# Optimization experiments

Measured on AMD Instinct MI355X. Metric: run time of the kernel, lower is better.

The kernel has to match this reference:

```python
import jax, jax.numpy as jnp
import numpy as np

N_HEADS = 16

def setup_inputs() -> dict:
    key = jax.random.key(0)
    ks = jax.random.split(key, 6)
    B, L, D = 1, 2048, 1024
    M = 2048  # max_len
    dh = D // N_HEADS
    s = 0.02
    return {
        "x": jax.random.normal(ks[0], (B, L, D), jnp.float32),
        "Wqkv": jax.random.normal(ks[1], (D, 3 * D), jnp.float32) * s,
        "bqkv": jax.random.normal(ks[2], (3 * D,), jnp.float32) * s,
        "Wout": jax.random.normal(ks[3], (D, D), jnp.float32) * s,
        "bout": jax.random.normal(ks[4], (D,), jnp.float32) * s,
        "rel_emb": jax.random.normal(ks[5], (2 * M - 1, dh), jnp.float32),
    }

def reference(x, Wqkv, bqkv, Wout, bout, rel_emb):
    B, L, D = x.shape
    H = N_HEADS
    dh = D // H
    qkv = x @ Wqkv + bqkv                       # [B,L,3D]
    q, k, v = jnp.split(qkv, 3, axis=-1)
    q = q.reshape(B, L, H, dh).transpose(0, 2, 1, 3)  # [B,H,L,dh]
    k = k.reshape(B, L, H, dh).transpose(0, 2, 1, 3)
    v = v.reshape(B, L, H, dh).transpose(0, 2, 1, 3)
    content = jnp.einsum('bhid,bhjd->bhij', q, k)      # [B,H,L,L]
    rel = jnp.einsum('bhid,rd->bhir', q, rel_emb)      # [B,H,L,2M-1]
    # _skew: F.pad(x,(1,0)); view keeps shape; slice [...,:L]
    rel = jnp.pad(rel, ((0, 0), (0, 0), (0, 0), (1, 0)))[..., :L]
    scores = (content + rel) / jnp.sqrt(jnp.asarray(dh, x.dtype))
    attn = jax.nn.softmax(scores, axis=-1)
    out = jnp.einsum('bhij,bhjd->bhid', attn, v)       # [B,H,L,dh]
    out = out.transpose(0, 2, 1, 3).reshape(B, L, D)
    return out @ Wout + bout
```

## Files before the change

### kernel.cpp

```cpp
#include <hip/hip_runtime.h>
#include <hip/hip_bf16.h>
#include <stdint.h>

typedef __attribute__((ext_vector_type(8))) __bf16 bf16x8;
typedef __attribute__((ext_vector_type(4))) float f32x4;
typedef __attribute__((ext_vector_type(16))) float f32x16;
typedef __attribute__((ext_vector_type(2))) uint32_t u32x2;

#define MFMA16(a, b, c) __builtin_amdgcn_mfma_f32_16x16x32_bf16(a, b, c, 0, 0, 0)
#define MFMA32(a, b, c) __builtin_amdgcn_mfma_f32_32x32x16_bf16(a, b, c, 0, 0, 0)

typedef const __attribute__((address_space(1))) uint32_t* gas_ptr;
typedef __attribute__((address_space(3))) uint32_t* lds_ptr;

static __device__ __forceinline__ ushort f2b(float f) {
  union { float f; uint32_t u; } x; x.f = f;
  uint32_t u = x.u + 0x7fffu + ((x.u >> 16) & 1u);
  return (ushort)(u >> 16);
}

static __device__ __forceinline__ void g2lds16(const void* g, void* l) {
  __builtin_amdgcn_global_load_lds((gas_ptr)(uintptr_t)g, (lds_ptr)(uintptr_t)l, 16, 0, 0);
}

template <int N> static __device__ __forceinline__ void waitvm() {
  if constexpr (N == 0) asm volatile("s_waitcnt vmcnt(0)" ::: "memory");
  else if constexpr (N == 4) asm volatile("s_waitcnt vmcnt(4)" ::: "memory");
  else if constexpr (N == 6) asm volatile("s_waitcnt vmcnt(6)" ::: "memory");
  else if constexpr (N == 8) asm volatile("s_waitcnt vmcnt(8)" ::: "memory");
}

static __device__ __forceinline__ u32x2 plswap(uint32_t a, uint32_t b) {
  return __builtin_amdgcn_permlane32_swap(a, b, false, false);
}
static __device__ __forceinline__ float xhalf_max(float x) {
  u32x2 r = plswap(__float_as_uint(x), __float_as_uint(x));
  return fmaxf(__uint_as_float(r.x), __uint_as_float(r.y));
}
static __device__ __forceinline__ float xhalf_sum(float x) {
  u32x2 r = plswap(__float_as_uint(x), __float_as_uint(x));
  return __uint_as_float(r.x) + __uint_as_float(r.y);
}

__global__ __launch_bounds__(256) void prep(const float* __restrict__ x, ushort* __restrict__ xb,
                                            const float* __restrict__ Wqkv, ushort* __restrict__ w1t,
                                            const float* __restrict__ Wout, ushort* __restrict__ w2t,
                                            int L) {
  const int b = blockIdx.x, t = threadIdx.x;
  const int ncvt = (L * 1024) / (256 * 4);
  if (b < ncvt) {
    int i = (b * 256 + t) * 4;
    float4 v = *(const float4*)(x + i);
    ushort4 o;
    o.x = f2b(v.x); o.y = f2b(v.y); o.z = f2b(v.z); o.w = f2b(v.w);
    *(ushort4*)(xb + i) = o;
    return;
  }
  __shared__ ushort tile[64][65];
  const float* in; ushort* out; int N; int b2;
  const int K = 1024;
  if (b < ncvt + 768) { b2 = b - ncvt; N = 3072; in = Wqkv; out = w1t; }
  else                { b2 = b - ncvt - 768; N = 1024; in = Wout; out = w2t; }
  int nx = b2 % (N >> 6), ky = b2 / (N >> 6);
  int n0 = nx * 64, k0 = ky * 64;
#pragma unroll
  for (int i = 0; i < 16; ++i) {
    int idx = i * 256 + t;
    int r = idx >> 6, c = idx & 63;
    tile[r][c] = f2b(in[(size_t)(k0 + r) * N + n0 + c]);
  }
  __syncthreads();
#pragma unroll
  for (int i = 0; i < 16; ++i) {
    int idx = i * 256 + t;
    int r = idx >> 6, c = idx & 63;
    out[(size_t)(n0 + r) * K + k0 + c] = tile[c][r];
  }
}

template <int BM, int BN, bool BIAS>
__global__ __launch_bounds__(256) void gemm_dbuf(const ushort* __restrict__ A,
                                                 const ushort* __restrict__ Bt,
                                                 float* __restrict__ C,
                                                 const float* __restrict__ bias,
                                                 int M, int N, int K) {
  constexpr int WM = BM / 2, WN = BN / 2, MF = WM / 16, NF = WN / 16;
  constexpr int AI = BM / 32, BI = BN / 32;
  __shared__ ushort lA[2][BM * 64];
  __shared__ ushort lB[2][BN * 64];
  const int t = threadIdx.x, lane = t & 63;
  const int bm = blockIdx.y * BM, bn = blockIdx.x * BN;
  const int wid = t >> 6, wr = wid >> 1, wc = wid & 1;

  f32x4 acc[MF][NF] = {};

  auto STAGE = [&](int bb, int k0) {
#pragma unroll
    for (int i = 0; i < AI; ++i) {
      int ci = i * 256 + t;
      int r = ci >> 3, cs = ci & 7;
      int cg = (cs ^ (r & 7)) * 8;
      g2lds16(A + (size_t)(bm + r) * K + k0 + cg, (ushort*)lA[bb] + ci * 8);
    }
#pragma unroll
    for (int i = 0; i < BI; ++i) {
      int ci = i * 256 + t;
      int r = ci >> 3, cs = ci & 7;
      int cg = (cs ^ (r & 7)) * 8;
      g2lds16(Bt + (size_t)(bn + r) * K + k0 + cg, (ushort*)lB[bb] + ci * 8);
    }
  };

  STAGE(0, 0);
  const int NS = K >> 6;
  int buf = 0;
  for (int s = 0; s < NS; ++s) {
    if (s + 1 < NS) { STAGE(buf ^ 1, (s + 1) << 6); waitvm<AI + BI>(); }
    else            { waitvm<0>(); }
    __builtin_amdgcn_s_barrier();
    __builtin_amdgcn_sched_barrier(0);
#pragma unroll
    for (int kk = 0; kk < 2; ++kk) {
      bf16x8 af[MF], bfr[NF];
#pragma unroll
      for (int m = 0; m < MF; ++m) {
        int row = wr * WM + m * 16 + (lane & 15);
        int cb = kk * 64 + ((lane >> 4) << 4);
        int sw = cb ^ ((row & 7) << 4);
        af[m] = *(const bf16x8*)((const char*)lA[buf] + row * 128 + sw);
      }
#pragma unroll
      for (int n = 0; n < NF; ++n) {
        int row = wc * WN + n * 16 + (lane & 15);
        int cb = kk * 64 + ((lane >> 4) << 4);
        int sw = cb ^ ((row & 7) << 4);
        bfr[n] = *(const bf16x8*)((const char*)lB[buf] + row * 128 + sw);
      }
      __builtin_amdgcn_s_setprio(1);
#pragma unroll
      for (int m = 0; m < MF; ++m)
#pragma unroll
        for (int n = 0; n < NF; ++n) acc[m][n] = MFMA16(af[m], bfr[n], acc[m][n]);
      __builtin_amdgcn_s_setprio(0);
    }
    __builtin_amdgcn_s_barrier();
    __builtin_amdgcn_sched_barrier(0);
    buf ^= 1;
  }
#pragma unroll
  for (int m = 0; m < MF; ++m) {
#pragma unroll
    for (int n = 0; n < NF; ++n) {
      int col = bn + wc * WN + n * 16 + (lane & 15);
      float b = BIAS ? bias[col] : 0.f;
#pragma unroll
      for (int r = 0; r < 4; ++r) {
        int row = bm + wr * WM + m * 16 + ((lane >> 4) << 2) + r;
        C[(size_t)row * N + col] = acc[m][n][r] + b;
      }
    }
  }
}

__global__ __launch_bounds__(256) void gemm_qkv(const ushort* __restrict__ A,
                                                const ushort* __restrict__ Bt,
                                                const float* __restrict__ bqkv,
                                                const float* __restrict__ rel,
                                                ushort* __restrict__ Qs,
                                                ushort* __restrict__ Kp,
                                                ushort* __restrict__ Vt, int M) {
  __shared__ ushort lA[2][128 * 64];
  __shared__ ushort lB[2][128 * 64];
  const int K = 1024;
  const int t = threadIdx.x, lane = t & 63;
  const int bm = blockIdx.y * 128, bn = blockIdx.x * 128;
  const int wid = t >> 6, wr = wid >> 1, wc = wid & 1;

  f32x4 acc[4][4] = {};

  auto STAGE = [&](int bb, int k0) {
#pragma unroll
    for (int i = 0; i < 4; ++i) {
      int ci = i * 256 + t;
      int r = ci >> 3, cs = ci & 7;
      int cg = (cs ^ (r & 7)) * 8;
      g2lds16(A + (size_t)(bm + r) * K + k0 + cg, (ushort*)lA[bb] + ci * 8);
      g2lds16(Bt + (size_t)(bn + r) * K + k0 + cg, (ushort*)lB[bb] + ci * 8);
    }
  };

  STAGE(0, 0);
  int buf = 0;
  for (int s = 0; s < 16; ++s) {
    if (s + 1 < 16) { STAGE(buf ^ 1, (s + 1) << 6); waitvm<8>(); }
    else            { waitvm<0>(); }
    __builtin_amdgcn_s_barrier();
    __builtin_amdgcn_sched_barrier(0);
#pragma unroll
    for (int kk = 0; kk < 2; ++kk) {
      bf16x8 af[4], bfr[4];
#pragma unroll
      for (int m = 0; m < 4; ++m) {
        int row = wr * 64 + m * 16 + (lane & 15);
        int cb = kk * 64 + ((lane >> 4) << 4);
        int sw = cb ^ ((row & 7) << 4);
        af[m] = *(const bf16x8*)((const char*)lA[buf] + row * 128 + sw);
      }
#pragma unroll
      for (int n = 0; n < 4; ++n) {
        int row = wc * 64 + n * 16 + (lane & 15);
        int cb = kk * 64 + ((lane >> 4) << 4);
        int sw = cb ^ ((row & 7) << 4);
        bfr[n] = *(const bf16x8*)((const char*)lB[buf] + row * 128 + sw);
      }
      __builtin_amdgcn_s_setprio(1);
#pragma unroll
      for (int m = 0; m < 4; ++m)
#pragma unroll
        for (int n = 0; n < 4; ++n) acc[m][n] = MFMA16(af[m], bfr[n], acc[m][n]);
      __builtin_amdgcn_s_setprio(0);
    }
    __builtin_amdgcn_s_barrier();
    __builtin_amdgcn_sched_barrier(0);
    buf ^= 1;
  }

  const int sec = bn >> 10;
  const int cis_base = bn & 1023;
  if (sec < 2) {
    ushort* dst = (sec == 0) ? Qs : Kp;
    const float scale = (sec == 0) ? 0.18033688f : 1.0f;
#pragma unroll
    for (int m = 0; m < 4; ++m) {
#pragma unroll
      for (int n = 0; n < 4; ++n) {
        int cis = cis_base + wc * 64 + n * 16 + (lane & 15);
        int hh = cis >> 6, dd = cis & 63;
        float b = bqkv[sec * 1024 + cis];
#pragma unroll
        for (int r = 0; r < 4; ++r) {
          int row = bm + wr * 64 + m * 16 + ((lane >> 4) << 2) + r;
          float v = acc[m][n][r] + b;
          if (sec == 1 && row > 0) v += rel[(size_t)(row - 1) * 64 + dd];
          dst[((size_t)hh * M + row) * 64 + dd] = f2b(v * scale);
        }
      }
    }
  } else {
    char* tb = (char*)lA;
#pragma unroll
    for (int m = 0; m < 4; ++m) {
#pragma unroll
      for (int n = 0; n < 4; ++n) {
        int cl = wc * 64 + n * 16 + (lane & 15);
        int ll = wr * 64 + m * 16 + ((lane >> 4) << 2);
        float b = bqkv[2048 + cis_base + cl];
        ushort4 w4;
        w4.x = f2b(acc[m][n][0] + b);
        w4.y = f2b(acc[m][n][1] + b);
        w4.z = f2b(acc[m][n][2] + b);
        w4.w = f2b(acc[m][n][3] + b);
        *(ushort4*)(tb + cl * 256 + ((ll * 2) ^ ((cl & 15) << 4))) = w4;
      }
    }
    __syncthreads();
#pragma unroll
    for (int ps = 0; ps < 8; ++ps) {
      int cl = ps * 16 + (t >> 4);
      int chunk = t & 15;
      uint4 rv = *(const uint4*)(tb + cl * 256 + ((chunk * 16) ^ ((cl & 15) << 4)));
      *(uint4*)(Vt + (size_t)(cis_base + cl) * M + bm + chunk * 8) = rv;
    }
  }
}

__global__ __launch_bounds__(512) void attn8(const ushort* __restrict__ Qs,
                                             const ushort* __restrict__ Kp,
                                             const ushort* __restrict__ Vt,
                                             ushort* __restrict__ O, int L) {
  __shared__ char smem[69632];
  __shared__ float mls[4][2][32];
  const int bid = blockIdx.x;
  const int h = (bid & 7) * 2 + (bid >> 7);
  const int q0 = ((bid >> 3) & 15) * 128;
  const int t = threadIdx.x, lane = t & 63, w = t >> 6;
  const int qt = w & 3, ks = w >> 2;
  const int ql = lane & 31, hi = lane >> 5;
  const int sw = (ql & 7) << 4;
  const ushort* kh = Kp + (size_t)h * L * 64;
  const ushort* vh = Vt + (size_t)h * 64 * L;
  const int half = L >> 1;
  const int NT = half >> 6;

  bf16x8 qf[4];
  {
    const ushort* qrow = Qs + ((size_t)h * L + q0 + qt * 32 + ql) * 64 + hi * 8;
#pragma unroll
    for (int c = 0; c < 4; ++c) qf[c] = *(const bf16x8*)(qrow + c * 16);
  }

  f32x16 ot0 = {}, ot1 = {};
  float m = -1e30f, l = 0.f;

  auto STAGE = [&](int bb, int tt) {
    char* base = smem + bb * 32768;
#pragma unroll
    for (int s = 0; s < 2; ++s) {
      int kb = s * half + tt * 64;
      char* sb = base + s * 16384;
      {
        int key = t >> 3, pch = t & 7;
        g2lds16(kh + (((size_t)(kb + key)) << 6) + ((pch ^ (key & 7)) << 3), sb + t * 16);
      }
      {
        int d = t >> 3, pch = t & 7;
        g2lds16(vh + (size_t)d * L + kb + ((pch ^ (d & 7)) << 3), sb + 8192 + t * 16);
      }
    }
  };

  STAGE(0, 0);
  int buf = 0;
  for (int tt = 0; tt < NT; ++tt) {
    if (tt + 1 < NT) { STAGE(buf ^ 1, tt + 1); waitvm<4>(); }
    else             { waitvm<0>(); }
    __builtin_amdgcn_s_barrier();
    __builtin_amdgcn_sched_barrier(0);
    const char* kbuf = smem + buf * 32768 + ks * 16384;
    const char* vbuf = kbuf + 8192;
    f32x16 s0 = {}, s1 = {};
    __builtin_amdgcn_s_setprio(1);
#pragma unroll
    for (int c = 0; c < 4; ++c) {
      bf16x8 k0 = *(const bf16x8*)(kbuf + ql * 128 + (((2 * c + hi) << 4) ^ sw));
      bf16x8 k1 = *(const bf16x8*)(kbuf + (32 + ql) * 128 + (((2 * c + hi) << 4) ^ sw));
      s0 = MFMA32(k0, qf[c], s0);
      s1 = MFMA32(k1, qf[c], s1);
    }
    __builtin_amdgcn_s_setprio(0);
    float mx = fmaxf(s0[0], s1[0]);
#pragma unroll
    for (int i = 1; i < 16; ++i) mx = fmaxf(fmaxf(s0[i], s1[i]), mx);
    mx = xhalf_max(mx);
    if (!__all(mx - m <= 8.0f)) {
      float mn = fmaxf(m, mx);
      float sc = __builtin_amdgcn_exp2f(m - mn);
      m = mn;
      l *= sc;
      ot0 = ot0 * sc;
      ot1 = ot1 * sc;
    }
    float rs = 0.f;
#pragma unroll
    for (int tl = 0; tl < 2; ++tl) {
      f32x16 s = tl ? s1 : s0;
      float p[16];
      float r0 = 0.f, r1 = 0.f;
#pragma unroll
      for (int i = 0; i < 16; i += 2) {
        p[i] = __builtin_amdgcn_exp2f(s[i] - m);
        p[i + 1] = __builtin_amdgcn_exp2f(s[i + 1] - m);
        r0 += p[i];
        r1 += p[i + 1];
      }
      rs += r0 + r1;
      uint32_t a[8];
#pragma unroll
      for (int i = 0; i < 8; ++i) {
        uint32_t r;
        asm("v_cvt_pk_bf16_f32 %0, %1, %2" : "=v"(r) : "v"(p[2 * i]), "v"(p[2 * i + 1]));
        a[i] = r;
      }
      u32x2 s02 = plswap(a[0], a[2]);
      u32x2 s13 = plswap(a[1], a[3]);
      u32x2 s46 = plswap(a[4], a[6]);
      u32x2 s57 = plswap(a[5], a[7]);
      union { uint32_t u[4]; bf16x8 v; } b0, b1;
      b0.u[0] = s02.x; b0.u[1] = s13.x; b0.u[2] = s02.y; b0.u[3] = s13.y;
      b1.u[0] = s46.x; b1.u[1] = s57.x; b1.u[2] = s46.y; b1.u[3] = s57.y;
      bf16x8 v00 = *(const bf16x8*)(vbuf + ql * 128 + (((tl * 4 + hi) << 4) ^ sw));
      bf16x8 v01 = *(const bf16x8*)(vbuf + ql * 128 + (((tl * 4 + 2 + hi) << 4) ^ sw));
      bf16x8 v10 = *(const bf16x8*)(vbuf + (32 + ql) * 128 + (((tl * 4 + hi) << 4) ^ sw));
      bf16x8 v11 = *(const bf16x8*)(vbuf + (32 + ql) * 128 + (((tl * 4 + 2 + hi) << 4) ^ sw));
      __builtin_amdgcn_s_setprio(1);
      ot0 = MFMA32(v00, b0.v, ot0);
      ot0 = MFMA32(v01, b1.v, ot0);
      ot1 = MFMA32(v10, b0.v, ot1);
      ot1 = MFMA32(v11, b1.v, ot1);
      __builtin_amdgcn_s_setprio(0);
    }
    l += xhalf_sum(rs);
    __builtin_amdgcn_s_barrier();
    __builtin_amdgcn_sched_barrier(0);
    buf ^= 1;
  }

  float* part = (float*)smem;
  float* merged = (float*)(smem + 4 * 64 * 33 * 4);
  if (ks == 1) {
    if (hi == 0) { mls[qt][0][ql] = m; mls[qt][1][ql] = l; }
    float* pq = part + qt * 64 * 33;
#pragma unroll
    for (int r = 0; r < 16; ++r) {
      int d = (r & 3) + 8 * (r >> 2) + 4 * hi;
      pq[d * 33 + ql] = ot0[r];
      pq[(d + 32) * 33 + ql] = ot1[r];
    }
  }
  __syncthreads();
  if (ks == 0) {
    float m1 = mls[qt][0][ql], l1 = mls[qt][1][ql];
    float mg = fmaxf(m, m1);
    float e0 = __builtin_amdgcn_exp2f(m - mg);
    float e1 = __builtin_amdgcn_exp2f(m1 - mg);
    float inv = 1.0f / (l * e0 + l1 * e1);
    float* pq = part + qt * 64 * 33;
    float* mq = merged + qt * 32 * 68;
#pragma unroll
    for (int r = 0; r < 16; ++r) {
      int d = (r & 3) + 8 * (r >> 2) + 4 * hi;
      mq[ql * 68 + d] = (ot0[r] * e0 + pq[d * 33 + ql] * e1) * inv;
      mq[ql * 68 + 32 + d] = (ot1[r] * e0 + pq[(d + 32) * 33 + ql] * e1) * inv;
    }
  }
  __syncthreads();
#pragma unroll
  for (int pss = 0; pss < 2; ++pss) {
    int id = pss * 512 + t;
    int qt2 = id >> 8, row = (id >> 3) & 31, c8 = id & 7;
    const float* mq = merged + qt2 * 32 * 68 + row * 68 + c8 * 8;
    float4 f0 = *(const float4*)mq;
    float4 f1 = *(const float4*)(mq + 4);
    union { ushort us[8]; uint4 u4; } o;
    o.us[0] = f2b(f0.x); o.us[1] = f2b(f0.y); o.us[2] = f2b(f0.z); o.us[3] = f2b(f0.w);
    o.us[4] = f2b(f1.x); o.us[5] = f2b(f1.y); o.us[6] = f2b(f1.z); o.us[7] = f2b(f1.w);
    *(uint4*)(O + (size_t)(q0 + qt2 * 32 + row) * 1024 + h * 64 + c8 * 8) = o.u4;
  }
}

extern "C" void kernel_launch(void* const* d_in, const int* in_sizes, int n_in,
                              void* d_out, int out_size, void* d_ws, size_t ws_size,
                              hipStream_t stream) {
  (void)n_in; (void)out_size; (void)ws_size;
  const float* x    = (const float*)d_in[0];
  const float* Wqkv = (const float*)d_in[1];
  const float* bqkv = (const float*)d_in[2];
  const float* Wout = (const float*)d_in[3];
  const float* bout = (const float*)d_in[4];
  const float* rel  = (const float*)d_in[5];
  float* out = (float*)d_out;
  const int L = in_sizes[0] / 1024;

  char* ws = (char*)d_ws;
  const size_t MB = 1024 * 1024;
  ushort* xb  = (ushort*)(ws);
  ushort* w1t = (ushort*)(ws + 4 * MB);
  ushort* w2t = (ushort*)(ws + 10 * MB);
  ushort* Qsb = (ushort*)(ws + 36 * MB);
  ushort* Kpb = (ushort*)(ws + 40 * MB);
  ushort* Vtb = (ushort*)(ws + 44 * MB);
  ushort* Ob  = (ushort*)(ws + 48 * MB);

  prep<<<dim3((L * 1024) / 1024 + 768 + 256), 256, 0, stream>>>(x, xb, Wqkv, w1t, Wout, w2t, L);
  gemm_qkv<<<dim3(3072 / 128, L / 128), 256, 0, stream>>>(xb, w1t, bqkv, rel, Qsb, Kpb, Vtb, L);
  attn8<<<dim3((L / 128) * 16), 512, 0, stream>>>(Qsb, Kpb, Vtb, Ob, L);
  gemm_dbuf<128, 64, true><<<dim3(1024 / 64, L / 128), 256, 0, stream>>>(Ob, w2t, out, bout, L, 1024, 1024);
}
```

Baseline: 81.97 us.

## Split attention keys four ways with smaller query tiles and register-staged prefetch

The attention kernel now handles 64 queries per block instead of 128 and splits the key range into four spans instead of two, doubling the grid to fill more CUs. The double-buffered async global-to-LDS copies are replaced by a single LDS buffer, with the next tile prefetched into registers and written to LDS between two barriers. The final merge now combines four partial softmax states instead of two. This raises parallelism and occupancy (launch bounds 512,4) at the cost of more merge work, an extra barrier per iteration, and register pressure from the prefetch registers.

```diff
diff --git a/kernel.cpp b/kernel.cpp
--- a/kernel.cpp
+++ b/kernel.cpp
@@ -274,23 +274,23 @@
   }
 }
 
-__global__ __launch_bounds__(512) void attn8(const ushort* __restrict__ Qs,
-                                             const ushort* __restrict__ Kp,
-                                             const ushort* __restrict__ Vt,
-                                             ushort* __restrict__ O, int L) {
+__global__ __launch_bounds__(512, 4) void attn11(const ushort* __restrict__ Qs,
+                                                 const ushort* __restrict__ Kp,
+                                                 const ushort* __restrict__ Vt,
+                                                 ushort* __restrict__ O, int L) {
   __shared__ char smem[69632];
-  __shared__ float mls[4][2][32];
+  __shared__ float mls[2][4][2][32];
   const int bid = blockIdx.x;
-  const int h = (bid & 7) * 2 + (bid >> 7);
-  const int q0 = ((bid >> 3) & 15) * 128;
+  const int h = (bid & 7) * 2 + (bid >> 8);
+  const int q0 = ((bid >> 3) & 31) * 64;
   const int t = threadIdx.x, lane = t & 63, w = t >> 6;
-  const int qt = w & 3, ks = w >> 2;
+  const int qt = w & 1, ks = w >> 1;
   const int ql = lane & 31, hi = lane >> 5;
   const int sw = (ql & 7) << 4;
   const ushort* kh = Kp + (size_t)h * L * 64;
   const ushort* vh = Vt + (size_t)h * 64 * L;
-  const int half = L >> 1;
-  const int NT = half >> 6;
+  const int span = L >> 2;
+  const int NT = span >> 6;
 
   bf16x8 qf[4];
   {
@@ -302,31 +302,40 @@
   f32x16 ot0 = {}, ot1 = {};
   float m = -1e30f, l = 0.f;
 
-  auto STAGE = [&](int bb, int tt) {
-    char* base = smem + bb * 32768;
-#pragma unroll
-    for (int s = 0; s < 2; ++s) {
-      int kb = s * half + tt * 64;
-      char* sb = base + s * 16384;
-      {
-        int key = t >> 3, pch = t & 7;
-        g2lds16(kh + (((size_t)(kb + key)) << 6) + ((pch ^ (key & 7)) << 3), sb + t * 16);
-      }
-      {
-        int d = t >> 3, pch = t & 7;
-        g2lds16(vh + (size_t)d * L + kb + ((pch ^ (d & 7)) << 3), sb + 8192 + t * 16);
-      }
-    }
-  };
-
-  STAGE(0, 0);
-  int buf = 0;
+  const int key8 = t >> 3, pch = t & 7;
+
+#pragma unroll
+  for (int i = 0; i < 8; ++i) {
+    int s = i >> 1;
+    char* sb = smem + s * 16384;
+    if ((i & 1) == 0)
+      g2lds16(kh + (((size_t)(s * span + key8)) << 6) + ((pch ^ (key8 & 7)) << 3),
+              sb + t * 16);
+    else
+      g2lds16(vh + (size_t)key8 * L + s * span + ((pch ^ (key8 & 7)) << 3),
+              sb + 8192 + t * 16);
+  }
+  waitvm<0>();
+  __builtin_amdgcn_s_barrier();
+  __builtin_amdgcn_sched_barrier(0);
+
+  const int wchunk = (pch << 4) ^ ((key8 & 7) << 4);
+
   for (int tt = 0; tt < NT; ++tt) {
-    if (tt + 1 < NT) { STAGE(buf ^ 1, tt + 1); waitvm<4>(); }
-    else             { waitvm<0>(); }
-    __builtin_amdgcn_s_barrier();
-    __builtin_amdgcn_sched_barrier(0);
-    const char* kbuf = smem + buf * 32768 + ks * 16384;
+    uint4 ld[8];
+    const bool pf = (tt + 1 < NT);
+    if (pf) {
+#pragma unroll
+      for (int i = 0; i < 8; ++i) {
+        int s = i >> 1;
+        int kb = s * span + (tt + 1) * 64;
+        if ((i & 1) == 0)
+          ld[i] = *(const uint4*)(kh + (((size_t)(kb + key8)) << 6) + pch * 8);
+        else
+          ld[i] = *(const uint4*)(vh + (size_t)key8 * L + kb + pch * 8);
+      }
+    }
+    const char* kbuf = smem + ks * 16384;
     const char* vbuf = kbuf + 8192;
     f32x16 s0 = {}, s1 = {};
     __builtin_amdgcn_s_setprio(1);
@@ -390,16 +399,26 @@
       __builtin_amdgcn_s_setprio(0);
     }
     l += xhalf_sum(rs);
-    __builtin_amdgcn_s_barrier();
-    __builtin_amdgcn_sched_barrier(0);
-    buf ^= 1;
+    __syncthreads();
+    if (pf) {
+#pragma unroll
+      for (int i = 0; i < 8; ++i) {
+        int s = i >> 1;
+        char* sb = smem + s * 16384;
+        if ((i & 1) == 0)
+          *(uint4*)(sb + key8 * 128 + wchunk) = ld[i];
+        else
+          *(uint4*)(sb + 8192 + key8 * 128 + wchunk) = ld[i];
+      }
+    }
+    __syncthreads();
   }
 
   float* part = (float*)smem;
-  float* merged = (float*)(smem + 4 * 64 * 33 * 4);
-  if (ks == 1) {
-    if (hi == 0) { mls[qt][0][ql] = m; mls[qt][1][ql] = l; }
-    float* pq = part + qt * 64 * 33;
+  float* merged = (float*)(smem + 51200);
+  if (ks != 0) {
+    if (hi == 0) { mls[qt][ks][0][ql] = m; mls[qt][ks][1][ql] = l; }
+    float* pq = part + (size_t)(qt * 3 + (ks - 1)) * 64 * 33;
 #pragma unroll
     for (int r = 0; r < 16; ++r) {
       int d = (r & 3) + 8 * (r >> 2) + 4 * hi;
@@ -409,25 +428,31 @@
   }
   __syncthreads();
   if (ks == 0) {
-    float m1 = mls[qt][0][ql], l1 = mls[qt][1][ql];
-    float mg = fmaxf(m, m1);
+    float m1 = mls[qt][1][0][ql], m2 = mls[qt][2][0][ql], m3 = mls[qt][3][0][ql];
+    float l1 = mls[qt][1][1][ql], l2 = mls[qt][2][1][ql], l3 = mls[qt][3][1][ql];
+    float mg = fmaxf(fmaxf(m, m1), fmaxf(m2, m3));
     float e0 = __builtin_amdgcn_exp2f(m - mg);
     float e1 = __builtin_amdgcn_exp2f(m1 - mg);
-    float inv = 1.0f / (l * e0 + l1 * e1);
-    float* pq = part + qt * 64 * 33;
+    float e2 = __builtin_amdgcn_exp2f(m2 - mg);
+    float e3 = __builtin_amdgcn_exp2f(m3 - mg);
+    float inv = 1.0f / (l * e0 + l1 * e1 + l2 * e2 + l3 * e3);
+    const float* p1 = part + (size_t)(qt * 3 + 0) * 64 * 33;
+    const float* p2 = part + (size_t)(qt * 3 + 1) * 64 * 33;
+    const float* p3 = part + (size_t)(qt * 3 + 2) * 64 * 33;
     float* mq = merged + qt * 32 * 68;
 #pragma unroll
     for (int r = 0; r < 16; ++r) {
       int d = (r & 3) + 8 * (r >> 2) + 4 * hi;
-      mq[ql * 68 + d] = (ot0[r] * e0 + pq[d * 33 + ql] * e1) * inv;
-      mq[ql * 68 + 32 + d] = (ot1[r] * e0 + pq[(d + 32) * 33 + ql] * e1) * inv;
+      mq[ql * 68 + d] =
+          (ot0[r] * e0 + p1[d * 33 + ql] * e1 + p2[d * 33 + ql] * e2 + p3[d * 33 + ql] * e3) * inv;
+      mq[ql * 68 + 32 + d] =
+          (ot1[r] * e0 + p1[(d + 32) * 33 + ql] * e1 + p2[(d + 32) * 33 + ql] * e2 +
+           p3[(d + 32) * 33 + ql] * e3) * inv;
     }
   }
   __syncthreads();
-#pragma unroll
-  for (int pss = 0; pss < 2; ++pss) {
-    int id = pss * 512 + t;
-    int qt2 = id >> 8, row = (id >> 3) & 31, c8 = id & 7;
+  {
+    int qt2 = t >> 8, row = (t >> 3) & 31, c8 = t & 7;
     const float* mq = merged + qt2 * 32 * 68 + row * 68 + c8 * 8;
     float4 f0 = *(const float4*)mq;
     float4 f1 = *(const float4*)(mq + 4);
@@ -463,6 +488,6 @@
 
   prep<<<dim3((L * 1024) / 1024 + 768 + 256), 256, 0, stream>>>(x, xb, Wqkv, w1t, Wout, w2t, L);
   gemm_qkv<<<dim3(3072 / 128, L / 128), 256, 0, stream>>>(xb, w1t, bqkv, rel, Qsb, Kpb, Vtb, L);
-  attn8<<<dim3((L / 128) * 16), 512, 0, stream>>>(Qsb, Kpb, Vtb, Ob, L);
+  attn11<<<dim3((L / 64) * 16), 512, 0, stream>>>(Qsb, Kpb, Vtb, Ob, L);
   gemm_dbuf<128, 64, true><<<dim3(1024 / 64, L / 128), 256, 0, stream>>>(Ob, w2t, out, bout, L, 1024, 1024);
 }
```

Result: slower. 130.3 us (+59.0%).

## Split attention keys across two blocks and merge partials in a separate kernel

Applied to the files above, without the earlier changes.

The attention kernel now splits the key range into two segments handled by separate blocks, doubling the grid from 256 to 512 blocks. Each block writes unnormalized fp32 partial outputs plus per-row max and sum, and a new merge kernel combines the two segments and converts to bf16. The aim is better occupancy across the GPU's compute units. The cost is an extra kernel launch and the fp32 partial traffic, about 16 MB written and then read back.

```diff
diff --git a/kernel.cpp b/kernel.cpp
--- a/kernel.cpp
+++ b/kernel.cpp
@@ -274,23 +274,26 @@
   }
 }
 
-__global__ __launch_bounds__(512) void attn8(const ushort* __restrict__ Qs,
-                                             const ushort* __restrict__ Kp,
-                                             const ushort* __restrict__ Vt,
-                                             ushort* __restrict__ O, int L) {
+__global__ __launch_bounds__(512) void attn12(const ushort* __restrict__ Qs,
+                                              const ushort* __restrict__ Kp,
+                                              const ushort* __restrict__ Vt,
+                                              float* __restrict__ Opart,
+                                              float* __restrict__ ml, int L) {
   __shared__ char smem[69632];
   __shared__ float mls[4][2][32];
   const int bid = blockIdx.x;
-  const int h = (bid & 7) * 2 + (bid >> 7);
+  const int h = (bid & 7) * 2 + ((bid >> 7) & 1);
   const int q0 = ((bid >> 3) & 15) * 128;
+  const int kseg = bid >> 8;
   const int t = threadIdx.x, lane = t & 63, w = t >> 6;
   const int qt = w & 3, ks = w >> 2;
   const int ql = lane & 31, hi = lane >> 5;
   const int sw = (ql & 7) << 4;
   const ushort* kh = Kp + (size_t)h * L * 64;
   const ushort* vh = Vt + (size_t)h * 64 * L;
-  const int half = L >> 1;
-  const int NT = half >> 6;
+  const int span = L >> 2;
+  const int base_k = kseg * (L >> 1);
+  const int NT = span >> 6;
 
   bf16x8 qf[4];
   {
@@ -306,7 +309,7 @@
     char* base = smem + bb * 32768;
 #pragma unroll
     for (int s = 0; s < 2; ++s) {
-      int kb = s * half + tt * 64;
+      int kb = base_k + s * span + tt * 64;
       char* sb = base + s * 16384;
       {
         int key = t >> 3, pch = t & 7;
@@ -413,14 +416,19 @@
     float mg = fmaxf(m, m1);
     float e0 = __builtin_amdgcn_exp2f(m - mg);
     float e1 = __builtin_amdgcn_exp2f(m1 - mg);
-    float inv = 1.0f / (l * e0 + l1 * e1);
+    float lg = l * e0 + l1 * e1;
+    if (hi == 0) {
+      size_t rr = (size_t)(kseg * 16 + h) * L + q0 + qt * 32 + ql;
+      ml[rr * 2] = mg;
+      ml[rr * 2 + 1] = lg;
+    }
     float* pq = part + qt * 64 * 33;
     float* mq = merged + qt * 32 * 68;
 #pragma unroll
     for (int r = 0; r < 16; ++r) {
       int d = (r & 3) + 8 * (r >> 2) + 4 * hi;
-      mq[ql * 68 + d] = (ot0[r] * e0 + pq[d * 33 + ql] * e1) * inv;
-      mq[ql * 68 + 32 + d] = (ot1[r] * e0 + pq[(d + 32) * 33 + ql] * e1) * inv;
+      mq[ql * 68 + d] = ot0[r] * e0 + pq[d * 33 + ql] * e1;
+      mq[ql * 68 + 32 + d] = ot1[r] * e0 + pq[(d + 32) * 33 + ql] * e1;
     }
   }
   __syncthreads();
@@ -431,11 +439,39 @@
     const float* mq = merged + qt2 * 32 * 68 + row * 68 + c8 * 8;
     float4 f0 = *(const float4*)mq;
     float4 f1 = *(const float4*)(mq + 4);
-    union { ushort us[8]; uint4 u4; } o;
-    o.us[0] = f2b(f0.x); o.us[1] = f2b(f0.y); o.us[2] = f2b(f0.z); o.us[3] = f2b(f0.w);
-    o.us[4] = f2b(f1.x); o.us[5] = f2b(f1.y); o.us[6] = f2b(f1.z); o.us[7] = f2b(f1.w);
-    *(uint4*)(O + (size_t)(q0 + qt2 * 32 + row) * 1024 + h * 64 + c8 * 8) = o.u4;
-  }
+    float* dst = Opart + ((size_t)(kseg * 16 + h) * L + q0 + qt2 * 32 + row) * 64 + c8 * 8;
+    *(float4*)dst = f0;
+    *(float4*)(dst + 4) = f1;
+  }
+}
+
+__global__ __launch_bounds__(256) void merge2(const float* __restrict__ Opart,
+                                              const float* __restrict__ ml,
+                                              ushort* __restrict__ O, int L) {
+  int idx = blockIdx.x * 256 + threadIdx.x;
+  int c8 = idx & 7;
+  int row = idx >> 3;
+  int h = row >> 11, q = row & (L - 1);
+  float m0 = ml[(size_t)row * 2], l0 = ml[(size_t)row * 2 + 1];
+  float m1 = ml[((size_t)16 * L + row) * 2], l1 = ml[((size_t)16 * L + row) * 2 + 1];
+  float M = fmaxf(m0, m1);
+  float w0 = __builtin_amdgcn_exp2f(m0 - M);
+  float w1 = __builtin_amdgcn_exp2f(m1 - M);
+  float inv = 1.0f / (l0 * w0 + l1 * w1);
+  const float* p0 = Opart + (size_t)row * 64 + c8 * 8;
+  const float* p1 = Opart + ((size_t)16 * L + row) * 64 + c8 * 8;
+  float4 a0 = *(const float4*)p0, a1 = *(const float4*)(p0 + 4);
+  float4 b0 = *(const float4*)p1, b1 = *(const float4*)(p1 + 4);
+  union { ushort us[8]; uint4 u4; } o;
+  o.us[0] = f2b((a0.x * w0 + b0.x * w1) * inv);
+  o.us[1] = f2b((a0.y * w0 + b0.y * w1) * inv);
+  o.us[2] = f2b((a0.z * w0 + b0.z * w1) * inv);
+  o.us[3] = f2b((a0.w * w0 + b0.w * w1) * inv);
+  o.us[4] = f2b((a1.x * w0 + b1.x * w1) * inv);
+  o.us[5] = f2b((a1.y * w0 + b1.y * w1) * inv);
+  o.us[6] = f2b((a1.z * w0 + b1.z * w1) * inv);
+  o.us[7] = f2b((a1.w * w0 + b1.w * w1) * inv);
+  *(uint4*)(O + (size_t)q * 1024 + h * 64 + c8 * 8) = o.u4;
 }
 
 extern "C" void kernel_launch(void* const* d_in, const int* in_sizes, int n_in,
@@ -453,16 +489,19 @@
 
   char* ws = (char*)d_ws;
   const size_t MB = 1024 * 1024;
-  ushort* xb  = (ushort*)(ws);
-  ushort* w1t = (ushort*)(ws + 4 * MB);
-  ushort* w2t = (ushort*)(ws + 10 * MB);
-  ushort* Qsb = (ushort*)(ws + 36 * MB);
-  ushort* Kpb = (ushort*)(ws + 40 * MB);
-  ushort* Vtb = (ushort*)(ws + 44 * MB);
-  ushort* Ob  = (ushort*)(ws + 48 * MB);
+  ushort* xb    = (ushort*)(ws);
+  ushort* w1t   = (ushort*)(ws + 4 * MB);
+  ushort* w2t   = (ushort*)(ws + 10 * MB);
+  float*  Opart = (float*)(ws + 12 * MB);
+  float*  mlb   = (float*)(ws + 28 * MB);
+  ushort* Qsb   = (ushort*)(ws + 36 * MB);
+  ushort* Kpb   = (ushort*)(ws + 40 * MB);
+  ushort* Vtb   = (ushort*)(ws + 44 * MB);
+  ushort* Ob    = (ushort*)(ws + 48 * MB);
 
   prep<<<dim3((L * 1024) / 1024 + 768 + 256), 256, 0, stream>>>(x, xb, Wqkv, w1t, Wout, w2t, L);
   gemm_qkv<<<dim3(3072 / 128, L / 128), 256, 0, stream>>>(xb, w1t, bqkv, rel, Qsb, Kpb, Vtb, L);
-  attn8<<<dim3((L / 128) * 16), 512, 0, stream>>>(Qsb, Kpb, Vtb, Ob, L);
+  attn12<<<dim3((L / 128) * 16 * 2), 512, 0, stream>>>(Qsb, Kpb, Vtb, Opart, mlb, L);
+  merge2<<<dim3(16 * L * 8 / 256), 256, 0, stream>>>(Opart, mlb, Ob, L);
   gemm_dbuf<128, 64, true><<<dim3(1024 / 64, L / 128), 256, 0, stream>>>(Ob, w2t, out, bout, L, 1024, 1024);
 }
```

Result: slower. 91.57 us (+11.7%).
